# Kernel optimization log

Hardware: AMD Instinct MI355X
Metric: run time of the kernel (lower is better)

The kernel has to match this reference:

```python
import jax, jax.numpy as jnp
import numpy as np

B, S, IN, OUT = 4, 2048, 4096, 4096


def setup_inputs() -> dict:
    key = jax.random.key(0)
    kx, kw, kb = jax.random.split(key, 3)
    x = jax.random.randint(kx, (B, S, IN), -127, 128, dtype=jnp.int8)
    weight = jax.random.randint(kw, (OUT, IN), -127, 128, dtype=jnp.int8)
    # original module initializes bias to zeros(int32); use random int32 to exercise the add
    bias = jax.random.randint(kb, (1, OUT), -1000, 1000, dtype=jnp.int32)
    return {"x": x, "weight": weight, "bias": bias}


def reference(x, weight, bias):
    x_shape = x.shape
    x2 = x.reshape(-1, x_shape[-1])  # [tokens, IN], int8
    # dot_general with preferred_element_type=int32 -> int8 inputs, int32 accumulate
    y = jax.lax.dot_general(
        x2, weight,
        dimension_numbers=(((1,), (1,)), ((), ())),
        preferred_element_type=jnp.int32,
    )  # [tokens, OUT] int32
    y = y + bias  # broadcast [1, OUT] int32
    return y.reshape(*x_shape[:-1], -1)
```

## Files before the change

### kernel.cpp

```cpp
#include <hip/hip_runtime.h>
#include <stdint.h>

#define M_TOT 8192
#define N_TOT 4096
#define K_TOT 4096

typedef int v4i  __attribute__((ext_vector_type(4)));
typedef int v16i __attribute__((ext_vector_type(16)));

__device__ __forceinline__ void gload_lds16(const void* g, void* l) {
    __builtin_amdgcn_global_load_lds(
        (const __attribute__((address_space(1))) unsigned int*)g,
        (__attribute__((address_space(3))) unsigned int*)l,
        16, 0, 0);
}

#define WAIT_V2_L0() __builtin_amdgcn_s_waitcnt(0x0072)
#define WAIT_V0_L0() __builtin_amdgcn_s_waitcnt(0x0070)
#define WAIT_V4()    __builtin_amdgcn_s_waitcnt(0x0f74)
#define SBAR()       __builtin_amdgcn_s_barrier()
#define SFENCE()     __builtin_amdgcn_sched_barrier(0)

__global__ __launch_bounds__(256) void pack2(
        const int4* __restrict__ xs, int4* __restrict__ xd,
        const int4* __restrict__ ws, int4* __restrict__ wd) {
    const int t = blockIdx.x * 256 + threadIdx.x;
#pragma unroll
    for (int it = 0; it < 6; ++it) {
        const long g = (long)it * 524288 + t;
        const int4* __restrict__ src = (it < 4) ? xs : ws;
        int4* __restrict__ dst       = (it < 4) ? xd : wd;
        const long o = (it < 4) ? g : g - 2097152;
        int4 r;
        int* rp = (int*)&r;
#pragma unroll
        for (int q = 0; q < 4; ++q) {
            const int4 a = src[o * 4 + q];
            rp[q] = (a.x & 255) | ((a.y & 255) << 8) |
                    ((a.z & 255) << 16) | (a.w << 24);
        }
        dst[o] = r;
    }
}

__global__ __launch_bounds__(512, 2) void i8gemm_bias(
        const signed char* __restrict__ x,
        const signed char* __restrict__ w,
        const int* __restrict__ bias,
        int* __restrict__ out) {
    __shared__ __align__(16) signed char la[3][256 * 64];
    __shared__ __align__(16) signed char lb[3][256 * 64];

    const int tid  = threadIdx.x;
    const int lane = tid & 63;
    const int wv   = tid >> 6;
    const int l31  = lane & 31;
    const int kh   = lane >> 5;
    const int wr   = wv >> 2;
    const int wc   = wv & 3;

    const int flat = blockIdx.y * gridDim.x + blockIdx.x;
    const int swz  = (flat & 7) * 64 + (flat >> 3);
    const int bn0  = (swz & 15) * 256;
    const int bm0  = (swz >> 4) * 256;

    int bv[2];
#pragma unroll
    for (int j = 0; j < 2; ++j) bv[j] = bias[bn0 + wc * 64 + j * 32 + l31];
    v16i acc[4][2];
#pragma unroll
    for (int i = 0; i < 4; ++i)
#pragma unroll
        for (int j = 0; j < 2; ++j)
#pragma unroll
            for (int r = 0; r < 16; ++r) acc[i][j][r] = bv[j];

    const int fc = (lane & 3) ^ ((lane >> 3) & 3);
    const signed char* pa = x + (long)(bm0 + wv * 32 + (lane >> 2)) * K_TOT + fc * 16;
    const signed char* pb = w + (long)(bn0 + wv * 32 + (lane >> 2)) * K_TOT + fc * 16;
    const int lbase = wv * 32 * 64;

    const int swr  = (l31 >> 1) & 3;
    const int aoff = (wr * 128 + l31) * 64;
    const int boff = (wc * 64  + l31) * 64;
    const int cs0  = ((kh    ) ^ swr) * 16;
    const int cs1  = ((2 + kh) ^ swr) * 16;

    signed char* A0 = &la[0][0]; signed char* A1 = &la[1][0]; signed char* A2 = &la[2][0];
    signed char* B0 = &lb[0][0]; signed char* B1 = &lb[1][0]; signed char* B2 = &lb[2][0];

#pragma unroll
    for (int i = 0; i < 2; ++i) {
        gload_lds16(pa + (long)i * 16 * K_TOT, A0 + lbase + i * 1024);
        gload_lds16(pb + (long)i * 16 * K_TOT, B0 + lbase + i * 1024);
    }
#pragma unroll
    for (int i = 0; i < 2; ++i) {
        gload_lds16(pa + 64 + (long)i * 16 * K_TOT, A1 + lbase + i * 1024);
        gload_lds16(pb + 64 + (long)i * 16 * K_TOT, B1 + lbase + i * 1024);
    }
    WAIT_V4();
    SBAR();
    SFENCE();

    v4i a0[4], b0[2], a1[4], b1[2];
#pragma unroll
    for (int i = 0; i < 4; ++i) a0[i] = *(const v4i*)(A0 + aoff + i * 2048 + cs0);
#pragma unroll
    for (int j = 0; j < 2; ++j) b0[j] = *(const v4i*)(B0 + boff + j * 2048 + cs0);

    const int NT = K_TOT / 64;
    for (int kt = 0; kt < NT; ++kt) {
        SFENCE();
#pragma unroll
        for (int i = 0; i < 4; ++i) a1[i] = *(const v4i*)(A0 + aoff + i * 2048 + cs1);
#pragma unroll
        for (int j = 0; j < 2; ++j) b1[j] = *(const v4i*)(B0 + boff + j * 2048 + cs1);
        SFENCE();
        if (kt + 2 < NT) {
            const long k0 = (long)(kt + 2) * 64;
#pragma unroll
            for (int i = 0; i < 2; ++i)
                gload_lds16(pa + k0 + (long)i * 16 * K_TOT, A2 + lbase + i * 1024);
        }
        SFENCE();
        __builtin_amdgcn_s_setprio(1);
#pragma unroll
        for (int i = 0; i < 4; ++i)
#pragma unroll
            for (int j = 0; j < 2; ++j)
                acc[i][j] = __builtin_amdgcn_mfma_i32_32x32x32_i8(
                    a0[i], b0[j], acc[i][j], 0, 0, 0);
        __builtin_amdgcn_s_setprio(0);
        SFENCE();
        if (kt + 2 < NT) { WAIT_V2_L0(); } else { WAIT_V0_L0(); }
        SFENCE();
        SBAR();
        SFENCE();
        if (kt + 1 < NT) {
#pragma unroll
            for (int i = 0; i < 4; ++i) a0[i] = *(const v4i*)(A1 + aoff + i * 2048 + cs0);
#pragma unroll
            for (int j = 0; j < 2; ++j) b0[j] = *(const v4i*)(B1 + boff + j * 2048 + cs0);
        }
        SFENCE();
        if (kt + 2 < NT) {
            const long k0 = (long)(kt + 2) * 64;
#pragma unroll
            for (int i = 0; i < 2; ++i)
                gload_lds16(pb + k0 + (long)i * 16 * K_TOT, B2 + lbase + i * 1024);
        }
        SFENCE();
        __builtin_amdgcn_s_setprio(1);
#pragma unroll
        for (int i = 0; i < 4; ++i)
#pragma unroll
            for (int j = 0; j < 2; ++j)
                acc[i][j] = __builtin_amdgcn_mfma_i32_32x32x32_i8(
                    a1[i], b1[j], acc[i][j], 0, 0, 0);

        signed char* t;
        t = A0; A0 = A1; A1 = A2; A2 = t;
        t = B0; B0 = B1; B1 = B2; B2 = t;
    }

#pragma unroll
    for (int i = 0; i < 4; ++i) {
        const int mbase = bm0 + wr * 128 + i * 32 + 4 * kh;
#pragma unroll
        for (int j = 0; j < 2; ++j) {
            const int n = bn0 + wc * 64 + j * 32 + l31;
#pragma unroll
            for (int r = 0; r < 16; ++r) {
                const int m = mbase + (r & 3) + 8 * (r >> 2);
                out[(long)m * N_TOT + n] = acc[i][j][r];
            }
        }
    }
}

extern "C" void kernel_launch(void* const* d_in, const int* in_sizes, int n_in,
                              void* d_out, int out_size, void* d_ws, size_t ws_size,
                              hipStream_t stream) {
    const int* x32  = (const int*)d_in[0];
    const int* w32  = (const int*)d_in[1];
    const int* bias = (const int*)d_in[2];
    int*       out  = (int*)d_out;

    signed char* xp = (signed char*)d_ws;
    signed char* wp = (signed char*)d_ws + (size_t)M_TOT * K_TOT;

    pack2<<<2048, 256, 0, stream>>>((const int4*)x32, (int4*)xp,
                                    (const int4*)w32, (int4*)wp);

    dim3 grid(N_TOT / 256, M_TOT / 256);
    i8gemm_bias<<<grid, 512, 0, stream>>>(xp, wp, bias, out);
}
```

Measured before the change: 395.7 us.

## Load pre-shuffled B fragments directly from global into registers, bypassing LDS

The pack kernel now writes the weight matrix in an MFMA-fragment order so each lane can load its B operand straight from global memory into registers, which removes the B LDS buffers and their DMA traffic. The main loop is restructured into four quarter-steps per K tile, each with partial A LDS reads, one A DMA issue or B register prefetch, a barrier and four MFMAs, unrolled by two to ping-pong the B registers. The aim is to halve LDS traffic and footprint. In exchange it adds many more barriers, and the global B loads have no explicit waitcnt before use, so their latency may be exposed.

```diff
diff --git a/kernel.cpp b/kernel.cpp
--- a/kernel.cpp
+++ b/kernel.cpp
@@ -15,41 +15,52 @@
         16, 0, 0);
 }
 
-#define WAIT_V2_L0() __builtin_amdgcn_s_waitcnt(0x0072)
-#define WAIT_V0_L0() __builtin_amdgcn_s_waitcnt(0x0070)
-#define WAIT_V4()    __builtin_amdgcn_s_waitcnt(0x0f74)
-#define SBAR()       __builtin_amdgcn_s_barrier()
-#define SFENCE()     __builtin_amdgcn_sched_barrier(0)
+#define WAIT_V6()  __builtin_amdgcn_s_waitcnt(0x0f76)
+#define SBAR()     __builtin_amdgcn_s_barrier()
+#define SFENCE()   __builtin_amdgcn_sched_barrier(0)
+#define MM(A, B, C) __builtin_amdgcn_mfma_i32_32x32x32_i8((A), (B), (C), 0, 0, 0)
 
 __global__ __launch_bounds__(256) void pack2(
         const int4* __restrict__ xs, int4* __restrict__ xd,
         const int4* __restrict__ ws, int4* __restrict__ wd) {
     const int t = blockIdx.x * 256 + threadIdx.x;
 #pragma unroll
-    for (int it = 0; it < 6; ++it) {
-        const long g = (long)it * 524288 + t;
-        const int4* __restrict__ src = (it < 4) ? xs : ws;
-        int4* __restrict__ dst       = (it < 4) ? xd : wd;
-        const long o = (it < 4) ? g : g - 2097152;
-        int4 r;
-        int* rp = (int*)&r;
+    for (int it = 0; it < 4; ++it) {
+        const long o = (long)it * 524288 + t;
+        int4 r; int* rp = (int*)&r;
 #pragma unroll
         for (int q = 0; q < 4; ++q) {
-            const int4 a = src[o * 4 + q];
+            const int4 a = xs[o * 4 + q];
             rp[q] = (a.x & 255) | ((a.y & 255) << 8) |
                     ((a.z & 255) << 16) | (a.w << 24);
         }
-        dst[o] = r;
+        xd[o] = r;
+    }
+#pragma unroll
+    for (int it = 0; it < 2; ++it) {
+        const int q   = it * 524288 + t;
+        const int l   = q & 31;
+        const int s   = (q >> 5) & 7;
+        const int ktb = (q >> 8) & 31;
+        const int nb  = q >> 13;
+        const long src = (long)(nb * 32 + l) * 1024 + ktb * 32 + s * 4;
+        int4 r; int* rp = (int*)&r;
+#pragma unroll
+        for (int qq = 0; qq < 4; ++qq) {
+            const int4 a = ws[src + qq];
+            rp[qq] = (a.x & 255) | ((a.y & 255) << 8) |
+                     ((a.z & 255) << 16) | (a.w << 24);
+        }
+        wd[q] = r;
     }
 }
 
 __global__ __launch_bounds__(512, 2) void i8gemm_bias(
         const signed char* __restrict__ x,
-        const signed char* __restrict__ w,
+        const signed char* __restrict__ wshuf,
         const int* __restrict__ bias,
         int* __restrict__ out) {
     __shared__ __align__(16) signed char la[3][256 * 64];
-    __shared__ __align__(16) signed char lb[3][256 * 64];
 
     const int tid  = threadIdx.x;
     const int lane = tid & 63;
@@ -77,92 +88,97 @@
 
     const int fc = (lane & 3) ^ ((lane >> 3) & 3);
     const signed char* pa = x + (long)(bm0 + wv * 32 + (lane >> 2)) * K_TOT + fc * 16;
-    const signed char* pb = w + (long)(bn0 + wv * 32 + (lane >> 2)) * K_TOT + fc * 16;
-    const int lbase = wv * 32 * 64;
+    const int sdst = wv * 32 * 64;
 
     const int swr  = (l31 >> 1) & 3;
     const int aoff = (wr * 128 + l31) * 64;
-    const int boff = (wc * 64  + l31) * 64;
-    const int cs0  = ((kh    ) ^ swr) * 16;
+    const int cs0  = ((0 + kh) ^ swr) * 16;
     const int cs1  = ((2 + kh) ^ swr) * 16;
-
-    signed char* A0 = &la[0][0]; signed char* A1 = &la[1][0]; signed char* A2 = &la[2][0];
-    signed char* B0 = &lb[0][0]; signed char* B1 = &lb[1][0]; signed char* B2 = &lb[2][0];
-
-#pragma unroll
-    for (int i = 0; i < 2; ++i) {
-        gload_lds16(pa + (long)i * 16 * K_TOT, A0 + lbase + i * 1024);
-        gload_lds16(pb + (long)i * 16 * K_TOT, B0 + lbase + i * 1024);
-    }
-#pragma unroll
-    for (int i = 0; i < 2; ++i) {
-        gload_lds16(pa + 64 + (long)i * 16 * K_TOT, A1 + lbase + i * 1024);
-        gload_lds16(pb + 64 + (long)i * 16 * K_TOT, B1 + lbase + i * 1024);
-    }
-    WAIT_V4();
+#define RD_A(T, i, cs) (*(const v4i*)((T) + aoff + (i) * 2048 + (cs)))
+
+    const int nbB = (bn0 >> 5) + wc * 2;
+    const signed char* qb0 = wshuf + (long)nbB * 131072 + lane * 16;
+    const signed char* qb1 = qb0 + 131072;
+
+    signed char* T0 = &la[0][0]; signed char* T1 = &la[1][0]; signed char* T2 = &la[2][0];
+
+    gload_lds16(pa,                 T0 + sdst);
+    gload_lds16(pa + 16L * K_TOT,   T0 + sdst + 1024);
+    gload_lds16(pa + 64,            T1 + sdst);
+    gload_lds16(pa + 64 + 16L * K_TOT, T1 + sdst + 1024);
+    SFENCE();
+    v4i bc0[2], bc1[2], bn0r[2], bn1r[2];
+    bc0[0] = *(const v4i*)(qb0);        bc0[1] = *(const v4i*)(qb1);
+    bc1[0] = *(const v4i*)(qb0 + 1024); bc1[1] = *(const v4i*)(qb1 + 1024);
+    qb0 += 2048; qb1 += 2048;
+    SFENCE();
+    WAIT_V6();
     SBAR();
     SFENCE();
 
-    v4i a0[4], b0[2], a1[4], b1[2];
-#pragma unroll
-    for (int i = 0; i < 4; ++i) a0[i] = *(const v4i*)(A0 + aoff + i * 2048 + cs0);
-#pragma unroll
-    for (int j = 0; j < 2; ++j) b0[j] = *(const v4i*)(B0 + boff + j * 2048 + cs0);
-
+    v4i a0[4], a1[4];
     const int NT = K_TOT / 64;
-    for (int kt = 0; kt < NT; ++kt) {
-        SFENCE();
-#pragma unroll
-        for (int i = 0; i < 4; ++i) a1[i] = *(const v4i*)(A0 + aoff + i * 2048 + cs1);
-#pragma unroll
-        for (int j = 0; j < 2; ++j) b1[j] = *(const v4i*)(B0 + boff + j * 2048 + cs1);
-        SFENCE();
-        if (kt + 2 < NT) {
-            const long k0 = (long)(kt + 2) * 64;
-#pragma unroll
-            for (int i = 0; i < 2; ++i)
-                gload_lds16(pa + k0 + (long)i * 16 * K_TOT, A2 + lbase + i * 1024);
-        }
-        SFENCE();
-        __builtin_amdgcn_s_setprio(1);
-#pragma unroll
-        for (int i = 0; i < 4; ++i)
-#pragma unroll
-            for (int j = 0; j < 2; ++j)
-                acc[i][j] = __builtin_amdgcn_mfma_i32_32x32x32_i8(
-                    a0[i], b0[j], acc[i][j], 0, 0, 0);
-        __builtin_amdgcn_s_setprio(0);
-        SFENCE();
-        if (kt + 2 < NT) { WAIT_V2_L0(); } else { WAIT_V0_L0(); }
-        SFENCE();
-        SBAR();
-        SFENCE();
-        if (kt + 1 < NT) {
-#pragma unroll
-            for (int i = 0; i < 4; ++i) a0[i] = *(const v4i*)(A1 + aoff + i * 2048 + cs0);
-#pragma unroll
-            for (int j = 0; j < 2; ++j) b0[j] = *(const v4i*)(B1 + boff + j * 2048 + cs0);
-        }
-        SFENCE();
-        if (kt + 2 < NT) {
-            const long k0 = (long)(kt + 2) * 64;
-#pragma unroll
-            for (int i = 0; i < 2; ++i)
-                gload_lds16(pb + k0 + (long)i * 16 * K_TOT, B2 + lbase + i * 1024);
-        }
-        SFENCE();
-        __builtin_amdgcn_s_setprio(1);
-#pragma unroll
-        for (int i = 0; i < 4; ++i)
-#pragma unroll
-            for (int j = 0; j < 2; ++j)
-                acc[i][j] = __builtin_amdgcn_mfma_i32_32x32x32_i8(
-                    a1[i], b1[j], acc[i][j], 0, 0, 0);
-
-        signed char* t;
-        t = A0; A0 = A1; A1 = A2; A2 = t;
-        t = B0; B0 = B1; B1 = B2; B2 = t;
-    }
+
+#define TILE(BC0, BC1, BN0, BN1, KT)                                        \
+do {                                                                        \
+    const long kdma = (long)((KT) + 2) * 64;                                \
+                                                                   \
+    a0[0] = RD_A(T0, 0, cs0);  a0[1] = RD_A(T0, 1, cs0);                    \
+    if ((KT) + 2 < NT) gload_lds16(pa + kdma, T2 + sdst);                   \
+    SFENCE(); SBAR();                                                       \
+    __builtin_amdgcn_s_setprio(1);                                          \
+    acc[0][0] = MM(a0[0], BC0[0], acc[0][0]);                               \
+    acc[0][1] = MM(a0[0], BC0[1], acc[0][1]);                               \
+    acc[1][0] = MM(a0[1], BC0[0], acc[1][0]);                               \
+    acc[1][1] = MM(a0[1], BC0[1], acc[1][1]);                               \
+    __builtin_amdgcn_s_setprio(0);                                          \
+    SFENCE(); SBAR(); SFENCE();                                             \
+                                                                   \
+    a0[2] = RD_A(T0, 2, cs0);  a0[3] = RD_A(T0, 3, cs0);                    \
+    if ((KT) + 2 < NT) gload_lds16(pa + kdma + 16L * K_TOT,                 \
+                                   T2 + sdst + 1024);                       \
+    SFENCE(); SBAR();                                                       \
+    __builtin_amdgcn_s_setprio(1);                                          \
+    acc[2][0] = MM(a0[2], BC0[0], acc[2][0]);                               \
+    acc[2][1] = MM(a0[2], BC0[1], acc[2][1]);                               \
+    acc[3][0] = MM(a0[3], BC0[0], acc[3][0]);                               \
+    acc[3][1] = MM(a0[3], BC0[1], acc[3][1]);                               \
+    __builtin_amdgcn_s_setprio(0);                                          \
+    SFENCE(); SBAR(); SFENCE();                                             \
+                                                                   \
+    a1[0] = RD_A(T0, 0, cs1);  a1[1] = RD_A(T0, 1, cs1);                    \
+    if ((KT) + 1 < NT) { BN0[0] = *(const v4i*)(qb0);                       \
+                         BN0[1] = *(const v4i*)(qb1); }                     \
+    SFENCE(); SBAR();                                                       \
+    __builtin_amdgcn_s_setprio(1);                                          \
+    acc[0][0] = MM(a1[0], BC1[0], acc[0][0]);                               \
+    acc[0][1] = MM(a1[0], BC1[1], acc[0][1]);                               \
+    acc[1][0] = MM(a1[1], BC1[0], acc[1][0]);                               \
+    acc[1][1] = MM(a1[1], BC1[1], acc[1][1]);                               \
+    __builtin_amdgcn_s_setprio(0);                                          \
+    SFENCE(); SBAR(); SFENCE();                                             \
+                                                                   \
+    a1[2] = RD_A(T0, 2, cs1);  a1[3] = RD_A(T0, 3, cs1);                    \
+    if ((KT) + 1 < NT) { BN1[0] = *(const v4i*)(qb0 + 1024);                \
+                         BN1[1] = *(const v4i*)(qb1 + 1024);                \
+                         qb0 += 2048; qb1 += 2048; }                        \
+    SFENCE(); SBAR();                                                       \
+    __builtin_amdgcn_s_setprio(1);                                          \
+    acc[2][0] = MM(a1[2], BC1[0], acc[2][0]);                               \
+    acc[2][1] = MM(a1[2], BC1[1], acc[2][1]);                               \
+    acc[3][0] = MM(a1[3], BC1[0], acc[3][0]);                               \
+    acc[3][1] = MM(a1[3], BC1[1], acc[3][1]);                               \
+    __builtin_amdgcn_s_setprio(0);                                          \
+    SFENCE(); SBAR(); SFENCE();                                             \
+    { signed char* t_ = T0; T0 = T1; T1 = T2; T2 = t_; }                    \
+} while (0)
+
+    for (int kt = 0; kt < NT; kt += 2) {
+        TILE(bc0, bc1, bn0r, bn1r, kt);
+        TILE(bn0r, bn1r, bc0, bc1, kt + 1);
+    }
+#undef TILE
+#undef RD_A
 
 #pragma unroll
     for (int i = 0; i < 4; ++i) {
```

New measurement: 408.9 us. 3.3% more time.

## Shrink GEMM block tile to 256x128 with four waves for two blocks per CU

Applied to the files above, without the earlier changes.

Changes each block from a 256x256 tile with 8 waves to a 256x128 tile with 4 waves, doubling the grid and cutting LDS use so two blocks can share a CU. Load counts and vmcnt waits are adjusted to the new A/B load split, and the swizzle is remapped for the wider grid. The intent is to let independent blocks overlap their barrier and load stalls. The cost is lower per-block data reuse, which means more global and L2 traffic for A. It also resets wave priority at the end of each iteration.

```diff
diff --git a/kernel.cpp b/kernel.cpp
--- a/kernel.cpp
+++ b/kernel.cpp
@@ -15,9 +15,9 @@
         16, 0, 0);
 }
 
-#define WAIT_V2_L0() __builtin_amdgcn_s_waitcnt(0x0072)
+#define WAIT_V4_L0() __builtin_amdgcn_s_waitcnt(0x0074)
 #define WAIT_V0_L0() __builtin_amdgcn_s_waitcnt(0x0070)
-#define WAIT_V4()    __builtin_amdgcn_s_waitcnt(0x0f74)
+#define WAIT_V6()    __builtin_amdgcn_s_waitcnt(0x0f76)
 #define SBAR()       __builtin_amdgcn_s_barrier()
 #define SFENCE()     __builtin_amdgcn_sched_barrier(0)
 
@@ -43,26 +43,26 @@
     }
 }
 
-__global__ __launch_bounds__(512, 2) void i8gemm_bias(
+__global__ __launch_bounds__(256, 2) void i8gemm_bias(
         const signed char* __restrict__ x,
         const signed char* __restrict__ w,
         const int* __restrict__ bias,
         int* __restrict__ out) {
     __shared__ __align__(16) signed char la[3][256 * 64];
-    __shared__ __align__(16) signed char lb[3][256 * 64];
+    __shared__ __align__(16) signed char lb[3][128 * 64];
 
     const int tid  = threadIdx.x;
     const int lane = tid & 63;
     const int wv   = tid >> 6;
     const int l31  = lane & 31;
     const int kh   = lane >> 5;
-    const int wr   = wv >> 2;
-    const int wc   = wv & 3;
+    const int wr   = wv >> 1;
+    const int wc   = wv & 1;
 
     const int flat = blockIdx.y * gridDim.x + blockIdx.x;
-    const int swz  = (flat & 7) * 64 + (flat >> 3);
-    const int bn0  = (swz & 15) * 256;
-    const int bm0  = (swz >> 4) * 256;
+    const int swz  = (flat & 7) * 128 + (flat >> 3);
+    const int bn0  = (swz & 31) * 128;
+    const int bm0  = (swz >> 5) * 256;
 
     int bv[2];
 #pragma unroll
@@ -76,9 +76,10 @@
             for (int r = 0; r < 16; ++r) acc[i][j][r] = bv[j];
 
     const int fc = (lane & 3) ^ ((lane >> 3) & 3);
-    const signed char* pa = x + (long)(bm0 + wv * 32 + (lane >> 2)) * K_TOT + fc * 16;
+    const signed char* pa = x + (long)(bm0 + wv * 64 + (lane >> 2)) * K_TOT + fc * 16;
     const signed char* pb = w + (long)(bn0 + wv * 32 + (lane >> 2)) * K_TOT + fc * 16;
-    const int lbase = wv * 32 * 64;
+    const int lba = wv * 64 * 64;
+    const int lbb = wv * 32 * 64;
 
     const int swr  = (l31 >> 1) & 3;
     const int aoff = (wr * 128 + l31) * 64;
@@ -90,16 +91,18 @@
     signed char* B0 = &lb[0][0]; signed char* B1 = &lb[1][0]; signed char* B2 = &lb[2][0];
 
 #pragma unroll
-    for (int i = 0; i < 2; ++i) {
-        gload_lds16(pa + (long)i * 16 * K_TOT, A0 + lbase + i * 1024);
-        gload_lds16(pb + (long)i * 16 * K_TOT, B0 + lbase + i * 1024);
-    }
-#pragma unroll
-    for (int i = 0; i < 2; ++i) {
-        gload_lds16(pa + 64 + (long)i * 16 * K_TOT, A1 + lbase + i * 1024);
-        gload_lds16(pb + 64 + (long)i * 16 * K_TOT, B1 + lbase + i * 1024);
-    }
-    WAIT_V4();
+    for (int i = 0; i < 4; ++i)
+        gload_lds16(pa + (long)i * 16 * K_TOT, A0 + lba + i * 1024);
+#pragma unroll
+    for (int i = 0; i < 2; ++i)
+        gload_lds16(pb + (long)i * 16 * K_TOT, B0 + lbb + i * 1024);
+#pragma unroll
+    for (int i = 0; i < 4; ++i)
+        gload_lds16(pa + 64 + (long)i * 16 * K_TOT, A1 + lba + i * 1024);
+#pragma unroll
+    for (int i = 0; i < 2; ++i)
+        gload_lds16(pb + 64 + (long)i * 16 * K_TOT, B1 + lbb + i * 1024);
+    WAIT_V6();
     SBAR();
     SFENCE();
 
@@ -120,8 +123,8 @@
         if (kt + 2 < NT) {
             const long k0 = (long)(kt + 2) * 64;
 #pragma unroll
-            for (int i = 0; i < 2; ++i)
-                gload_lds16(pa + k0 + (long)i * 16 * K_TOT, A2 + lbase + i * 1024);
+            for (int i = 0; i < 4; ++i)
+                gload_lds16(pa + k0 + (long)i * 16 * K_TOT, A2 + lba + i * 1024);
         }
         SFENCE();
         __builtin_amdgcn_s_setprio(1);
@@ -133,7 +136,7 @@
                     a0[i], b0[j], acc[i][j], 0, 0, 0);
         __builtin_amdgcn_s_setprio(0);
         SFENCE();
-        if (kt + 2 < NT) { WAIT_V2_L0(); } else { WAIT_V0_L0(); }
+        if (kt + 2 < NT) { WAIT_V4_L0(); } else { WAIT_V0_L0(); }
         SFENCE();
         SBAR();
         SFENCE();
@@ -148,7 +151,7 @@
             const long k0 = (long)(kt + 2) * 64;
 #pragma unroll
             for (int i = 0; i < 2; ++i)
-                gload_lds16(pb + k0 + (long)i * 16 * K_TOT, B2 + lbase + i * 1024);
+                gload_lds16(pb + k0 + (long)i * 16 * K_TOT, B2 + lbb + i * 1024);
         }
         SFENCE();
         __builtin_amdgcn_s_setprio(1);
@@ -158,6 +161,7 @@
             for (int j = 0; j < 2; ++j)
                 acc[i][j] = __builtin_amdgcn_mfma_i32_32x32x32_i8(
                     a1[i], b1[j], acc[i][j], 0, 0, 0);
+        __builtin_amdgcn_s_setprio(0);
 
         signed char* t;
         t = A0; A0 = A1; A1 = A2; A2 = t;
@@ -193,6 +197,6 @@
     pack2<<<2048, 256, 0, stream>>>((const int4*)x32, (int4*)xp,
                                     (const int4*)w32, (int4*)wp);
 
-    dim3 grid(N_TOT / 256, M_TOT / 256);
-    i8gemm_bias<<<grid, 512, 0, stream>>>(xp, wp, bias, out);
-}
+    dim3 grid(N_TOT / 128, M_TOT / 256);
+    i8gemm_bias<<<grid, 256, 0, stream>>>(xp, wp, bias, out);
+}
```

Result: slower. 408.4 us (+3.2%).
